# Kernel optimization log

Hardware: AMD Instinct MI355X
Metric: run time of the kernel (lower is better)

## Reference

```python
import jax, jax.numpy as jnp
import numpy as np

NBATCH, NELEC, NATOMS, NBAS, NORB = 1024, 64, 16, 256, 128

# per-atom shell pattern: (l, m) pairs; bas_n = l (standard for GTO primitives)
_SHELL_LM = [(0, 0), (1, -1), (1, 0), (1, 1), (2, -2), (2, -1), (2, 0), (2, 1), (2, 2),
             (0, 0), (1, -1), (1, 0), (1, 1), (2, 0), (2, 2), (2, -2)]


def _norm_gaussian(bas_exp, bas_n):
    # Torch _norm_gaussian: bas_n += 1; A = exp**(0.25*(2n+1)); B = 2**(2n+1.5);
    # C = factorial2(2n-1)*sqrt(pi); norm = sqrt(B/C)*A
    n1 = bas_n + 1.0
    A = bas_exp ** (0.25 * (2.0 * n1 + 1.0))
    B = 2.0 ** (2.0 * n1 + 1.5)
    # 2*n1-1 in {1,3,5} for n in {0,1,2}: factorial2 -> {1,3,15}
    f2 = np.array([1.0, 3.0, 15.0], dtype=np.float32)[bas_n.astype(np.int32)]
    C = f2 * np.float32(np.sqrt(np.pi))
    return (np.sqrt(B / C) * A).astype(np.float32)


def setup_inputs() -> dict:
    key = jax.random.key(0)
    k0, k1, k2, k3, k4 = jax.random.split(key, 5)
    inp = jax.random.normal(k0, (NBATCH, NELEC, 3), jnp.float32) * 2.0
    atom_coords = jax.random.normal(k1, (NATOMS, 3), jnp.float32) * 3.0
    bas_exp = jax.random.uniform(k2, (NBAS,), jnp.float32, minval=0.2, maxval=3.0)
    bas_coeffs = jax.random.uniform(k3, (NBAS,), jnp.float32, minval=0.5, maxval=1.0)

    lm = np.array(_SHELL_LM * (NBAS // len(_SHELL_LM)), dtype=np.int32)  # [NBAS,2]
    bas_l = jnp.asarray(lm[:, 0])
    bas_m = jnp.asarray(lm[:, 1])
    bas_n = jnp.asarray(lm[:, 0].astype(np.float32))
    bas_atom_index = jnp.asarray((np.arange(NBAS) // (NBAS // NATOMS)).astype(np.int32))
    index_ctr = jnp.sort(jax.random.randint(k4, (NBAS,), 0, NORB)).astype(jnp.int32)
    norm_cst = jnp.asarray(_norm_gaussian(np.asarray(bas_exp), np.asarray(bas_n)))
    return {
        'input': inp, 'atom_coords': atom_coords, 'bas_exp': bas_exp,
        'bas_coeffs': bas_coeffs, 'norm_cst': norm_cst, 'bas_n': bas_n,
        'bas_l': bas_l, 'bas_m': bas_m, 'bas_atom_index': bas_atom_index,
        'index_ctr': index_ctr,
    }


def _spherical_harmonics(xyz, r, r2, bas_l, bas_m):
    # real spherical harmonics up to l=2 (QMCTorch constants)
    x, y, z = xyz[..., 0], xyz[..., 1], xyz[..., 2]
    C0 = 0.2820948          # 1/(2 sqrt(pi))
    C1 = 0.4886025          # sqrt(3/(4 pi))
    C2XY = 1.0925484        # sqrt(15/(4 pi))
    C2Z2 = 0.31539156       # sqrt(5/(16 pi))
    C2D = 0.5462742         # sqrt(15/(16 pi))
    y1 = C1 * jnp.where(bas_m == -1, y, jnp.where(bas_m == 0, z, x)) / r
    y2 = jnp.where(bas_m == -2, C2XY * x * y,
         jnp.where(bas_m == -1, C2XY * y * z,
         jnp.where(bas_m == 0, C2Z2 * (2.0 * z * z - x * x - y * y),
         jnp.where(bas_m == 1, C2XY * z * x, C2D * (x * x - y * y))))) / r2
    return jnp.where(bas_l == 0, C0, jnp.where(bas_l == 1, y1, y2))


def reference(input, atom_coords, bas_exp, bas_coeffs, norm_cst, bas_n,
              bas_l, bas_m, bas_atom_index, index_ctr):
    # bas_coords = atom_coords.repeat_interleave(nshells) expressed as a gather
    bas_coords = atom_coords[bas_atom_index]                     # [nbas, 3]
    xyz = input[:, :, None, :] - bas_coords[None, None, :, :]    # [B, E, nbas, 3]
    r2 = jnp.sum(xyz * xyz, axis=-1)                             # [B, E, nbas]
    r = jnp.sqrt(r2)
    R = r ** bas_n * jnp.exp(-bas_exp * r2)                      # gaussian radial
    Y = _spherical_harmonics(xyz, r, r2, bas_l, bas_m)
    bas = norm_cst * bas_coeffs * R * Y                          # [B, E, nbas]
    ao = jnp.zeros((input.shape[0], input.shape[1], NORB), bas.dtype)
    return ao.at[:, :, index_ctr].add(bas)                       # index_add over dim 2
```

## Files before the change

kernel.cpp:

```cpp
#include <hip/hip_runtime.h>

#define NBAS   256
#define NORB   128
#define NROWS  65536
#define RPB    16
#define NATOM  16
#define TSTR   12
#define PSTR   260

__device__ __forceinline__ float wave_scan_incl(float x) {
    int t;
    t = __builtin_amdgcn_update_dpp(0, __float_as_int(x), 0x111, 0xf, 0xf, false);
    x += __int_as_float(t);
    t = __builtin_amdgcn_update_dpp(0, __float_as_int(x), 0x112, 0xf, 0xf, false);
    x += __int_as_float(t);
    t = __builtin_amdgcn_update_dpp(0, __float_as_int(x), 0x114, 0xf, 0xf, false);
    x += __int_as_float(t);
    t = __builtin_amdgcn_update_dpp(0, __float_as_int(x), 0x118, 0xf, 0xf, false);
    x += __int_as_float(t);
    t = __builtin_amdgcn_update_dpp(0, __float_as_int(x), 0x142, 0xa, 0xf, false);
    x += __int_as_float(t);
    t = __builtin_amdgcn_update_dpp(0, __float_as_int(x), 0x143, 0xc, 0xf, false);
    x += __int_as_float(t);
    return x;
}

__global__ __launch_bounds__(256, 5) void ao_kernel(
    const float* __restrict__ inp,
    const float* __restrict__ atom_coords,
    const float* __restrict__ bas_exp,
    const float* __restrict__ bas_coeffs,
    const float* __restrict__ norm_cst,
    const int*   __restrict__ bas_l,
    const int*   __restrict__ bas_m,
    const int*   __restrict__ bas_atom_index,
    const int*   __restrict__ index_ctr,
    float* __restrict__ out)
{
    __shared__ __align__(16) float s_tab [4][4][NATOM][TSTR];
    __shared__ __align__(16) float s_pref[4][4][PSTR];
    __shared__ int s_start[NORB + 1];

    const int tid = threadIdx.x;
    const int w   = tid >> 6, ln = tid & 63;
    const int rowbase = (int)blockIdx.x * RPB + 4 * w;
    const int b4 = ln << 2;
    const int a4 = ln >> 2;

    const float4 vex = *reinterpret_cast<const float4*>(&bas_exp[b4]);
    const float4 vcf = *reinterpret_cast<const float4*>(&bas_coeffs[b4]);
    const float4 vnm = *reinterpret_cast<const float4*>(&norm_cst[b4]);
    const int4   vl  = *reinterpret_cast<const int4*>(&bas_l[b4]);
    const int4   vm  = *reinterpret_cast<const int4*>(&bas_m[b4]);
    const float exs[4] = {vex.x, vex.y, vex.z, vex.w};
    const float cfs[4] = {vcf.x*vnm.x, vcf.y*vnm.y, vcf.z*vnm.z, vcf.w*vnm.w};
    const int   ls[4]  = {vl.x, vl.y, vl.z, vl.w};
    const int   ms[4]  = {vm.x, vm.y, vm.z, vm.w};

    const float C0 = 0.2820948f, C1 = 0.4886025f, C2XY = 1.0925484f,
                C2Z2 = 0.31539156f, C2D = 0.5462742f;
    float nex[4], lcc[4];
    int   idxs[4];
    #pragma unroll
    for (int k = 0; k < 4; ++k) {
        int l = ls[k], m = ms[k], idx; float C;
        if (l == 0)      { idx = 0; C = C0; }
        else if (l == 1) { idx = (m == -1) ? 2 : (m == 0) ? 3 : 1; C = C1; }
        else {
            if      (m == -2) { idx = 4; C = C2XY; }
            else if (m == -1) { idx = 5; C = C2XY; }
            else if (m ==  0) { idx = 6; C = C2Z2; }
            else if (m ==  1) { idx = 7; C = C2XY; }
            else              { idx = 8; C = C2D;  }
        }
        nex[k]  = -exs[k] * 1.4426950408889634f;
        lcc[k]  = __log2f(cfs[k] * C);
        idxs[k] = idx;
    }

    {
        int ic   = index_ctr[tid];
        int prev = (tid == 0) ? -1 : index_ctr[tid - 1];
        for (int o = prev + 1; o <= ic; ++o) s_start[o] = tid;
        if (tid == NBAS - 1)
            for (int o = ic + 1; o <= NORB; ++o) s_start[o] = NBAS;
    }

    {
        const int r = ln >> 4, a = ln & 15;
        const int row = rowbase + r;
        float px = inp[row*3+0], py = inp[row*3+1], pz = inp[row*3+2];
        float x = px - atom_coords[a*3+0];
        float y = py - atom_coords[a*3+1];
        float z = pz - atom_coords[a*3+2];
        float x2 = x*x, y2 = y*y, z2 = z*z;
        float r2 = x2 + y2 + z2;
        float* e = &s_tab[w][r][a][0];
        reinterpret_cast<float4*>(e)[0] = make_float4(1.0f, x, y, z);
        reinterpret_cast<float4*>(e)[1] = make_float4(x*y, y*z, fmaf(3.f, z2, -r2), z*x);
        reinterpret_cast<float4*>(e)[2] = make_float4(x2 - y2, r2, 0.f, 0.f);
    }
    __syncthreads();

    const float* tb = &s_tab[w][0][a4][0];
    #pragma unroll
    for (int r = 0; r < 4; ++r) {
        const float* t = tb + r * (4 * NATOM * TSTR) / 4;
        float r2 = t[9];
        float ev[4];
        #pragma unroll
        for (int k = 0; k < 4; ++k)
            ev[k] = __builtin_exp2f(fmaf(nex[k], r2, lcc[k])) * t[idxs[k]];
        float e0 = ev[0];
        float e1 = e0 + ev[1];
        float e2 = e1 + ev[2];
        float e3 = e2 + ev[3];
        float s    = wave_scan_incl(e3);
        float excl = s - e3;
        *reinterpret_cast<float4*>(&s_pref[w][r][b4]) =
            make_float4(excl, excl + e0, excl + e1, excl + e2);
        if (ln == 63) s_pref[w][r][NBAS] = s;
    }

    const int q4 = (ln & 31) << 2;
    int st[5];
    #pragma unroll
    for (int k = 0; k < 5; ++k) st[k] = s_start[q4 + k];
    #pragma unroll
    for (int g = 0; g < 2; ++g) {
        const int row = 2*g + (ln >> 5);
        const float* pf = s_pref[w][row];
        float p0 = pf[st[0]], p1 = pf[st[1]], p2 = pf[st[2]],
              p3 = pf[st[3]], p4 = pf[st[4]];
        float4 o4 = make_float4(p1-p0, p2-p1, p3-p2, p4-p3);
        *reinterpret_cast<float4*>(&out[(size_t)(rowbase + row) * NORB + q4]) = o4;
    }
}

extern "C" void kernel_launch(void* const* d_in, const int* in_sizes, int n_in,
                              void* d_out, int out_size, void* d_ws, size_t ws_size,
                              hipStream_t stream) {
    const float* inp   = (const float*)d_in[0];
    const float* atomc = (const float*)d_in[1];
    const float* bexp  = (const float*)d_in[2];
    const float* bcoef = (const float*)d_in[3];
    const float* bnorm = (const float*)d_in[4];
    const int* bl   = (const int*)d_in[6];
    const int* bm   = (const int*)d_in[7];
    const int* bai  = (const int*)d_in[8];
    const int* ictr = (const int*)d_in[9];
    float* out = (float*)d_out;

    hipLaunchKernelGGL(ao_kernel, dim3(NROWS / RPB), dim3(256), 0, stream,
                       inp, atomc, bexp, bcoef, bnorm, bl, bm, bai, ictr, out);
}
```

Baseline: 21.71 us.

## Fuse per-row prefix gather into scan loop with single-row LDS buffer

The prefix-sum scratch buffer shrinks from four rows per wave to one row that is reused. Each row's output differences are gathered and stored as float2 right after that row's scan, so the separate output phase is gone. Spherical-harmonic index and constant selection becomes arithmetic, with the monomial table reordered to match, and launch bounds are raised so more blocks can fit per CU. The shared buffer is reused across rows inside a wave without an explicit barrier, which relies on in-order execution within the wave. The output stores are narrower (float2 instead of float4).

```diff
diff --git a/kernel.cpp b/kernel.cpp
--- a/kernel.cpp
+++ b/kernel.cpp
@@ -6,7 +6,7 @@
 #define RPB    16
 #define NATOM  16
 #define TSTR   12
-#define PSTR   260
+#define PSTR   264
 
 __device__ __forceinline__ float wave_scan_incl(float x) {
     int t;
@@ -25,7 +25,7 @@
     return x;
 }
 
-__global__ __launch_bounds__(256, 5) void ao_kernel(
+__global__ __launch_bounds__(256, 8) void ao_kernel(
     const float* __restrict__ inp,
     const float* __restrict__ atom_coords,
     const float* __restrict__ bas_exp,
@@ -38,7 +38,7 @@
     float* __restrict__ out)
 {
     __shared__ __align__(16) float s_tab [4][4][NATOM][TSTR];
-    __shared__ __align__(16) float s_pref[4][4][PSTR];
+    __shared__ __align__(16) float s_pref[4][PSTR];
     __shared__ int s_start[NORB + 1];
 
     const int tid = threadIdx.x;
@@ -63,16 +63,12 @@
     int   idxs[4];
     #pragma unroll
     for (int k = 0; k < 4; ++k) {
-        int l = ls[k], m = ms[k], idx; float C;
-        if (l == 0)      { idx = 0; C = C0; }
-        else if (l == 1) { idx = (m == -1) ? 2 : (m == 0) ? 3 : 1; C = C1; }
-        else {
-            if      (m == -2) { idx = 4; C = C2XY; }
-            else if (m == -1) { idx = 5; C = C2XY; }
-            else if (m ==  0) { idx = 6; C = C2Z2; }
-            else if (m ==  1) { idx = 7; C = C2XY; }
-            else              { idx = 8; C = C2D;  }
-        }
+        const int l = ls[k], m = ms[k];
+        const int idx = (l == 0) ? 0 : (m + 4*l - 2);
+        const float C = (idx == 0) ? C0
+                      : (idx <  4) ? C1
+                      : (idx == 6) ? C2Z2
+                      : (idx == 8) ? C2D : C2XY;
         nex[k]  = -exs[k] * 1.4426950408889634f;
         lcc[k]  = __log2f(cfs[k] * C);
         idxs[k] = idx;
@@ -96,44 +92,38 @@
         float x2 = x*x, y2 = y*y, z2 = z*z;
         float r2 = x2 + y2 + z2;
         float* e = &s_tab[w][r][a][0];
-        reinterpret_cast<float4*>(e)[0] = make_float4(1.0f, x, y, z);
+        reinterpret_cast<float4*>(e)[0] = make_float4(1.0f, y, z, x);
         reinterpret_cast<float4*>(e)[1] = make_float4(x*y, y*z, fmaf(3.f, z2, -r2), z*x);
         reinterpret_cast<float4*>(e)[2] = make_float4(x2 - y2, r2, 0.f, 0.f);
     }
     __syncthreads();
 
     const float* tb = &s_tab[w][0][a4][0];
+    const float* pmono[4] = { tb + idxs[0], tb + idxs[1], tb + idxs[2], tb + idxs[3] };
+    const float* pr2 = tb + 9;
+    float* pf = s_pref[w];
+    const int st0 = s_start[2*ln], st1 = s_start[2*ln+1], st2 = s_start[2*ln+2];
+
     #pragma unroll
     for (int r = 0; r < 4; ++r) {
-        const float* t = tb + r * (4 * NATOM * TSTR) / 4;
-        float r2 = t[9];
+        const int roff = r * NATOM * TSTR;
+        float r2 = pr2[roff];
         float ev[4];
         #pragma unroll
         for (int k = 0; k < 4; ++k)
-            ev[k] = __builtin_exp2f(fmaf(nex[k], r2, lcc[k])) * t[idxs[k]];
+            ev[k] = __builtin_exp2f(fmaf(nex[k], r2, lcc[k])) * pmono[k][roff];
         float e0 = ev[0];
         float e1 = e0 + ev[1];
         float e2 = e1 + ev[2];
         float e3 = e2 + ev[3];
         float s    = wave_scan_incl(e3);
         float excl = s - e3;
-        *reinterpret_cast<float4*>(&s_pref[w][r][b4]) =
+        *reinterpret_cast<float4*>(&pf[b4]) =
             make_float4(excl, excl + e0, excl + e1, excl + e2);
-        if (ln == 63) s_pref[w][r][NBAS] = s;
-    }
-
-    const int q4 = (ln & 31) << 2;
-    int st[5];
-    #pragma unroll
-    for (int k = 0; k < 5; ++k) st[k] = s_start[q4 + k];
-    #pragma unroll
-    for (int g = 0; g < 2; ++g) {
-        const int row = 2*g + (ln >> 5);
-        const float* pf = s_pref[w][row];
-        float p0 = pf[st[0]], p1 = pf[st[1]], p2 = pf[st[2]],
-              p3 = pf[st[3]], p4 = pf[st[4]];
-        float4 o4 = make_float4(p1-p0, p2-p1, p3-p2, p4-p3);
-        *reinterpret_cast<float4*>(&out[(size_t)(rowbase + row) * NORB + q4]) = o4;
+        if (ln == 63) pf[NBAS] = s;
+        float p0 = pf[st0], p1 = pf[st1], p2 = pf[st2];
+        *reinterpret_cast<float2*>(&out[(size_t)(rowbase + r) * NORB + 2*ln]) =
+            make_float2(p1 - p0, p2 - p1);
     }
 }
 
```

Measured after the change: 19.15 us. 11.8% less time.
